# Performance work log

Measured on AMD Instinct MI355X. Metric: run time of the kernel, lower is better.

## Reference

```python
import jax, jax.numpy as jnp
import numpy as np

B, C, H, W = 1, 256, 48, 64
HW = H * W
HIDDEN, CTX = 128, 64
LEVELS, RADIUS = 4, 4
WIN = 2 * RADIUS + 1
P = WIN * WIN                     # 81 lookup points per level
CORR_DIM = P * LEVELS             # 324
TOP_K = 3
ITERS = 4
STEP_ROT, STEP_TRANS = 0.02, 0.02


def _sample_templates():
    # 12 directions x 3 scales + identity = 37 pose perturbations (as in __init__)
    base = [([0,0,0],[1,0,0]),([0,0,0],[-1,0,0]),([0,0,0],[0,1,0]),([0,0,0],[0,-1,0]),
            ([0,0,0],[0,0,1]),([0,0,0],[0,0,-1]),([1,0,0],[0,0,0]),([-1,0,0],[0,0,0]),
            ([0,1,0],[0,0,0]),([0,-1,0],[0,0,0]),([0,0,1],[0,0,0]),([0,0,-1],[0,0,0])]
    scales = np.array([0.25, 1.0, 4.0], np.float32)
    rot = np.repeat(np.array([r for r, _ in base], np.float32), 3, axis=0)
    trs = np.repeat(np.array([t for _, t in base], np.float32), 3, axis=0)
    sc = np.tile(scales, 12)
    axes = rot / np.clip(np.linalg.norm(rot, axis=1, keepdims=True), 1e-8, None)
    ha = STEP_ROT * sc / 2.0
    dq = np.stack([np.cos(ha), axes[:, 0]*np.sin(ha), axes[:, 1]*np.sin(ha), axes[:, 2]*np.sin(ha)], -1)
    dt = trs * (STEP_TRANS * sc[:, None])
    dq = np.concatenate([dq, [[1., 0., 0., 0.]]], 0)
    dt = np.concatenate([dt, [[0., 0., 0.]]], 0)
    return jnp.asarray(dq), jnp.asarray(dt)

DQ, DT = _sample_templates()     # (37,4), (37,3)
N_SAMPLES = DQ.shape[0]


def qmul(q, r):
    w1, x1, y1, z1 = jnp.moveaxis(q, -1, 0)
    w2, x2, y2, z2 = jnp.moveaxis(r, -1, 0)
    return jnp.stack([w1*w2 - x1*x2 - y1*y2 - z1*z2,
                      w1*x2 + x1*w2 + y1*z2 - z1*y2,
                      w1*y2 - x1*z2 + y1*w2 + z1*x2,
                      w1*z2 + x1*y2 - y1*x2 + z1*w2], -1)


def qapply(q, v):
    qv = jnp.concatenate([jnp.zeros(v.shape[:-1] + (1,), v.dtype), v], -1)
    qc = q * jnp.array([1., -1., -1., -1.], q.dtype)
    return qmul(qmul(q, qv), qc)[..., 1:]


def quat_to_R(q):
    w, x, y, z = jnp.moveaxis(q, -1, 0)
    R = jnp.stack([1-2*(y*y+z*z), 2*(x*y-w*z), 2*(x*z+w*y),
                   2*(x*y+w*z), 1-2*(x*x+z*z), 2*(y*z-w*x),
                   2*(x*z-w*y), 2*(y*z+w*x), 1-2*(x*x+y*y)], -1)
    return R.reshape(q.shape[:-1] + (3, 3))


def conv3(x, w, b):
    y = jax.lax.conv_general_dilated(x, w, (1, 1), 'SAME',
                                     dimension_numbers=('NCHW', 'OIHW', 'NCHW'))
    return y + b[None, :, None, None]


def bilinear_lookup(corr_flat, Hl, Wl, x, y):
    # corr_flat: (B,HW,Hl*Wl); x,y: (B,N,HW,P) -> (B,N,HW,P), zero padding outside
    x0 = jnp.floor(x)
    y0 = jnp.floor(y)
    out = jnp.zeros(x.shape, corr_flat.dtype)
    def gather(idx):
        g = lambda ix: jnp.take_along_axis(corr_flat, ix, axis=-1)
        return jax.vmap(g, in_axes=1, out_axes=1)(idx)   # vmap over N, no corr copy
    for dx_, dy_ in ((0, 0), (1, 0), (0, 1), (1, 1)):
        xi = x0 + dx_
        yi = y0 + dy_
        wgt = (1 - jnp.abs(x - xi)) * (1 - jnp.abs(y - yi))
        valid = (xi >= 0) & (xi < Wl) & (yi >= 0) & (yi < Hl)
        idx = (jnp.clip(yi, 0, Hl - 1) * Wl + jnp.clip(xi, 0, Wl - 1)).astype(jnp.int32)
        out = out + jnp.where(valid, wgt, 0.0) * gather(idx)
    return out


def _forward(fmap_rgb, fmap_depth, depth, context, intrinsics,
             Wz, bz, Wr, br, Wq, bq, Wh, bh, Wfc, bfc):
    f32 = jnp.float32
    fx = 60. + 40. * intrinsics[:, 0]
    fy = 60. + 40. * intrinsics[:, 1]
    cx = W / 2. + 4. * (intrinsics[:, 2] - 0.5)
    cy = H / 2. + 4. * (intrinsics[:, 3] - 0.5)
    d = 4.0 + 20.0 * depth                                  # (B,H,W) metric depth

    # 4D correlation pyramid: corr[b,i,:,:] = <fmap_depth pixel i, fmap_rgb>
    fd = fmap_depth.reshape(B, C, HW).transpose(0, 2, 1)    # (B,HW,C)
    corr = jnp.einsum('bic,bchw->bihw', fd, fmap_rgb) / jnp.sqrt(f32(C))
    pyramid = []
    cl, Hl, Wl = corr, H, W
    for _ in range(LEVELS):
        pyramid.append((cl.reshape(B, HW, Hl * Wl), Hl, Wl))
        cl = cl.reshape(B, HW, Hl // 2, 2, Wl // 2, 2).mean(axis=(3, 5))
        Hl //= 2
        Wl //= 2

    # back-projected depth points (B,HW,3)
    vv, uu = jnp.meshgrid(jnp.arange(H, dtype=f32), jnp.arange(W, dtype=f32), indexing='ij')
    uu = uu.reshape(HW)
    vv = vv.reshape(HW)
    df = d.reshape(B, HW)
    X = jnp.stack([(uu[None] - cx[:, None]) / fx[:, None] * df,
                   (vv[None] - cy[:, None]) / fy[:, None] * df, df], -1)

    off = jnp.arange(-RADIUS, RADIUS + 1, dtype=f32)
    oy, ox = jnp.meshgrid(off, off, indexing='ij')
    ox = ox.reshape(P)
    oy = oy.reshape(P)

    pose = jnp.tile(jnp.array([1., 0., 0., 0., 0., 0., 0.], f32)[None, :], (B, 1))
    h = jnp.zeros((B, HIDDEN, H, W), f32)

    for _ in range(ITERS):
        qc, tc = pose[:, :4], pose[:, 4:7]
        quats = qmul(qc[:, None, :], DQ[None])              # (B,N,4)
        quats = quats / jnp.linalg.norm(quats, axis=-1, keepdims=True)
        trans = tc[:, None, :] + qapply(qc[:, None, :], DT[None])
        Rm = quat_to_R(quats)                               # (B,N,3,3)
        Xc = jnp.einsum('bnij,bpj->bnpi', Rm, X) + trans[:, :, None, :]
        z = jnp.clip(Xc[..., 2], 0.1, None)
        u = fx[:, None, None] * Xc[..., 0] / z + cx[:, None, None]   # (B,N,HW)
        v = fy[:, None, None] * Xc[..., 1] / z + cy[:, None, None]
        feats = []
        for lvl, (cfl, Hl_, Wl_) in enumerate(pyramid):
            s = f32(2 ** lvl)
            xl = u[..., None] / s + ox
            yl = v[..., None] / s + oy
            feats.append(bilinear_lookup(cfl, Hl_, Wl_, xl, yl))
        cf = jnp.concatenate(feats, -1)                     # (B,N,HW,CORR_DIM)
        conf = cf.mean(axis=(2, 3))                         # (B,N) sample confidence
        topv, topi = jax.lax.top_k(conf, TOP_K)
        wk = jax.nn.softmax(topv, axis=-1)                  # confidence-weighted top-K
        idx = jnp.broadcast_to(topi[:, :, None, None], (B, TOP_K, HW, CORR_DIM))
        sel = jnp.take_along_axis(cf, idx, axis=1)
        fused = (wk[:, :, None, None] * sel).sum(1)         # (B,HW,CORR_DIM)
        fused = fused.transpose(0, 2, 1).reshape(B, CORR_DIM, H, W)

        # ConvGRU update
        x_in = jnp.concatenate([fused, context], 1)
        hx = jnp.concatenate([h, x_in], 1)
        zg = jax.nn.sigmoid(conv3(hx, Wz, bz))
        rg = jax.nn.sigmoid(conv3(hx, Wr, br))
        qg = jnp.tanh(conv3(jnp.concatenate([rg * h, x_in], 1), Wq, bq))
        h = (1 - zg) * h + zg * qg

        # 7D pose delta head + quaternion/Lie-style update
        feat = jax.nn.relu(conv3(h, Wh, bh)).mean(axis=(2, 3))
        delta = 0.01 * (feat @ Wfc + bfc)                   # (B,7)
        dq = jnp.concatenate([1.0 + delta[:, :1], delta[:, 1:4]], -1)
        dq = dq / jnp.linalg.norm(dq, axis=-1, keepdims=True)
        tn = tc + qapply(qc, delta[:, 4:7])
        qn = qmul(qc, dq)
        qn = qn / jnp.linalg.norm(qn, axis=-1, keepdims=True)
        pose = jnp.concatenate([qn, tn], -1)
    return pose


def setup_inputs() -> dict:
    key = jax.random.key(0)
    ks = jax.random.split(key, 12)
    rn = lambda k, shape, s=1.0: s * jax.random.normal(k, shape, jnp.float32)
    Gin = HIDDEN + CORR_DIM + CTX
    sc = 1.0 / np.sqrt(Gin * 9)
    sh = 1.0 / np.sqrt(HIDDEN * 9)
    return {
        'fmap_rgb': rn(ks[0], (B, C, H, W)),
        'fmap_depth': rn(ks[1], (B, C, H, W)),
        'depth': jax.random.uniform(ks[2], (B, H, W), jnp.float32),
        'context': rn(ks[3], (B, CTX, H, W)),
        'intrinsics': jax.random.uniform(ks[4], (B, 4), jnp.float32),
        'Wz': rn(ks[5], (HIDDEN, Gin, 3, 3), sc), 'bz': jnp.zeros((HIDDEN,), jnp.float32),
        'Wr': rn(ks[6], (HIDDEN, Gin, 3, 3), sc), 'br': jnp.zeros((HIDDEN,), jnp.float32),
        'Wq': rn(ks[7], (HIDDEN, Gin, 3, 3), sc), 'bq': jnp.zeros((HIDDEN,), jnp.float32),
        'Wh': rn(ks[8], (HIDDEN, HIDDEN, 3, 3), sh), 'bh': jnp.zeros((HIDDEN,), jnp.float32),
        'Wfc': rn(ks[9], (HIDDEN, 7), 1.0 / np.sqrt(HIDDEN)), 'bfc': jnp.zeros((7,), jnp.float32),
    }


def reference(fmap_rgb, fmap_depth, depth, context, intrinsics,
              Wz, bz, Wr, br, Wq, bq, Wh, bh, Wfc, bfc):
    return _forward(fmap_rgb, fmap_depth, depth, context, intrinsics,
                    Wz, bz, Wr, br, Wq, bq, Wh, bh, Wfc, bfc)
```

## Files before the change

### kernel.cpp

```cpp
#include <hip/hip_runtime.h>
#include <math.h>

constexpr int kH = 48, kW = 64, kHW = 3072, kC = 256;
constexpr int kHidden = 128, kCtx = 64;
constexpr int kP = 81, kCorrDim = 324;
constexpr int kNS = 37, kIters = 4;
constexpr int kGin = kHidden + kCorrDim + kCtx;
constexpr int kCinPad = 544;
constexpr int kStepsBig = 17 * 9;
constexpr int kStepsH = 4 * 9;

constexpr int kSB0 = 0, kSB1 = 4292, kSB2 = 5720, kSB3 = 6292, kSBTot = 6580;
constexpr int kHB0 = 0, kHB1 = 3552, kHB2 = 4560, kHB3 = 4872, kHBTot = 4980;

constexpr size_t U_CORR0 = 0;
constexpr size_t U_CORR1 = U_CORR0 + (size_t)kHW * 3072;
constexpr size_t U_CORR2 = U_CORR1 + (size_t)kHW * 768;
constexpr size_t U_CORR3 = U_CORR2 + (size_t)kHW * 192;
constexpr size_t U_END0  = U_CORR3 + (size_t)kHW * 48;
constexpr size_t F_X     = U_END0 / 2;
constexpr size_t F_H     = F_X + (size_t)kHW * 3;
constexpr size_t F_ZPRE  = F_H + (size_t)kHidden * kHW;
constexpr size_t F_END1  = F_ZPRE + (size_t)kHidden * kHW;
constexpr size_t U_BUFT  = F_END1 * 2;
constexpr size_t U_RHT   = U_BUFT + (size_t)kHW * kCinPad;
constexpr size_t U_PZR   = U_RHT + (size_t)kHW * kHidden;
constexpr size_t U_PQ    = U_PZR + (size_t)kStepsBig * 256 * 32;
constexpr size_t U_PH    = U_PQ + (size_t)kStepsBig * 128 * 32;
constexpr size_t U_END2  = U_PH + (size_t)kStepsH * 128 * 32;
constexpr size_t F_BZR   = (U_END2 + 2) / 2;
constexpr size_t F_CONF  = F_BZR + 256;
constexpr size_t F_TK    = F_CONF + 64;
constexpr size_t F_POSE  = F_TK + 16;
constexpr size_t F_FEAT  = F_POSE + 16;
constexpr size_t F_END3  = F_FEAT + 128;
constexpr size_t U_FDT   = F_END3 * 2;
constexpr size_t U_QT    = U_FDT + (size_t)kHW * kC;
constexpr size_t U_SBOX  = U_FDT;

typedef __attribute__((ext_vector_type(8))) short short8;
typedef __attribute__((ext_vector_type(4))) float f32x4;

__device__ inline unsigned short f2b(float f) {
  unsigned int u = __float_as_uint(f);
  unsigned int r = u + 0x7FFF + ((u >> 16) & 1);
  return (unsigned short)(r >> 16);
}
__device__ inline float b2f(unsigned short u) {
  return __uint_as_float(((unsigned int)u) << 16);
}
__device__ inline int clampi(int v, int lo, int hi) { return min(max(v, lo), hi); }

__constant__ float c_rot[12][3] = {
  {0,0,0},{0,0,0},{0,0,0},{0,0,0},{0,0,0},{0,0,0},
  {1,0,0},{-1,0,0},{0,1,0},{0,-1,0},{0,0,1},{0,0,-1}};
__constant__ float c_trs[12][3] = {
  {1,0,0},{-1,0,0},{0,1,0},{0,-1,0},{0,0,1},{0,0,-1},
  {0,0,0},{0,0,0},{0,0,0},{0,0,0},{0,0,0},{0,0,0}};

__device__ inline void d_qmul(const float* q, const float* r, float* o) {
  o[0] = q[0]*r[0] - q[1]*r[1] - q[2]*r[2] - q[3]*r[3];
  o[1] = q[0]*r[1] + q[1]*r[0] + q[2]*r[3] - q[3]*r[2];
  o[2] = q[0]*r[2] - q[1]*r[3] + q[2]*r[0] + q[3]*r[1];
  o[3] = q[0]*r[3] + q[1]*r[2] - q[2]*r[1] + q[3]*r[0];
}
__device__ inline void d_qapply(const float* q, const float* v, float* o) {
  float a0 = -q[1]*v[0] - q[2]*v[1] - q[3]*v[2];
  float a1 =  q[0]*v[0] + q[2]*v[2] - q[3]*v[1];
  float a2 =  q[0]*v[1] - q[1]*v[2] + q[3]*v[0];
  float a3 =  q[0]*v[2] + q[1]*v[1] - q[2]*v[0];
  o[0] = -a0*q[1] + a1*q[0] - a2*q[3] + a3*q[2];
  o[1] = -a0*q[2] + a1*q[3] + a2*q[0] - a3*q[1];
  o[2] = -a0*q[3] - a1*q[2] + a2*q[1] + a3*q[0];
}
__device__ inline void d_intr(const float* intr, float& fx, float& fy, float& cx, float& cy) {
  fx = 60.f + 40.f*intr[0];
  fy = 60.f + 40.f*intr[1];
  cx = 32.f + 4.f*(intr[2] - 0.5f);
  cy = 24.f + 4.f*(intr[3] - 0.5f);
}
__device__ inline void sample_Rt(int t, const float* __restrict__ pose, float* S) {
  float qc[4] = {pose[0], pose[1], pose[2], pose[3]};
  float tc[3] = {pose[4], pose[5], pose[6]};
  float dq[4], dt[3];
  if (t == 36) {
    dq[0] = 1.f; dq[1] = dq[2] = dq[3] = 0.f;
    dt[0] = dt[1] = dt[2] = 0.f;
  } else {
    int j = t / 3, k = t % 3;
    float sc = (k == 0) ? 0.25f : ((k == 1) ? 1.f : 4.f);
    float rx = c_rot[j][0], ry = c_rot[j][1], rz = c_rot[j][2];
    float nrm = sqrtf(rx*rx + ry*ry + rz*rz);
    float axn = fmaxf(nrm, 1e-8f);
    float ax = rx / axn, ay = ry / axn, az = rz / axn;
    float ha = 0.02f * sc * 0.5f;
    float sh = sinf(ha), ch = cosf(ha);
    dq[0] = ch; dq[1] = ax * sh; dq[2] = ay * sh; dq[3] = az * sh;
    dt[0] = c_trs[j][0] * (0.02f * sc);
    dt[1] = c_trs[j][1] * (0.02f * sc);
    dt[2] = c_trs[j][2] * (0.02f * sc);
  }
  float qn[4];
  d_qmul(qc, dq, qn);
  float inv = 1.f / sqrtf(qn[0]*qn[0] + qn[1]*qn[1] + qn[2]*qn[2] + qn[3]*qn[3]);
  qn[0] *= inv; qn[1] *= inv; qn[2] *= inv; qn[3] *= inv;
  float tr[3];
  d_qapply(qc, dt, tr);
  float w = qn[0], x = qn[1], y = qn[2], z = qn[3];
  S[0] = 1.f - 2.f*(y*y + z*z); S[1] = 2.f*(x*y - w*z);       S[2] = 2.f*(x*z + w*y);
  S[3] = 2.f*(x*y + w*z);       S[4] = 1.f - 2.f*(x*x + z*z); S[5] = 2.f*(y*z - w*x);
  S[6] = 2.f*(x*z - w*y);       S[7] = 2.f*(y*z + w*x);       S[8] = 1.f - 2.f*(x*x + y*y);
  S[9]  = tc[0] + tr[0];
  S[10] = tc[1] + tr[1];
  S[11] = tc[2] + tr[2];
}
__device__ inline void project_uv(const float* S, const float* Xp, const float* intr,
                                  float& u, float& v) {
  float xc0 = S[0]*Xp[0] + S[1]*Xp[1] + S[2]*Xp[2] + S[9];
  float xc1 = S[3]*Xp[0] + S[4]*Xp[1] + S[5]*Xp[2] + S[10];
  float xc2 = S[6]*Xp[0] + S[7]*Xp[1] + S[8]*Xp[2] + S[11];
  float z = fmaxf(xc2, 0.1f);
  float fx, fy, cx, cy;
  d_intr(intr, fx, fy, cx, cy);
  u = fx * xc0 / z + cx;
  v = fy * xc1 / z + cy;
}

__global__ void init_k(const float* __restrict__ ctx, const float* __restrict__ bz,
                       const float* __restrict__ br, const float* __restrict__ depth,
                       const float* __restrict__ intr, float* __restrict__ h,
                       unsigned short* __restrict__ bufT, float* __restrict__ bzr,
                       float* __restrict__ X, float* __restrict__ conf,
                       float* __restrict__ feat, float* __restrict__ pose) {
  int idx = blockIdx.x * blockDim.x + threadIdx.x;
  if (idx < kHidden * kHW) {
    h[idx] = 0.f;
    int p = idx >> 7, c = idx & 127;
    bufT[(size_t)p * kCinPad + c] = 0;
  }
  if (idx < kHW * 92) {
    int p = idx / 92, c = idx % 92;
    unsigned short v = 0;
    if (c < 64) v = f2b(ctx[(size_t)c * kHW + p]);
    bufT[(size_t)p * kCinPad + 452 + c] = v;
  }
  if (idx < kHW) {
    float fx, fy, cx, cy;
    d_intr(intr, fx, fy, cx, cy);
    float d = 4.f + 20.f * depth[idx];
    float u = (float)(idx % kW), v = (float)(idx / kW);
    X[idx*3+0] = (u - cx) / fx * d;
    X[idx*3+1] = (v - cy) / fy * d;
    X[idx*3+2] = d;
  }
  if (idx < 256) bzr[idx] = (idx < 128) ? bz[idx] : br[idx - 128];
  if (idx < 64) conf[idx] = 0.f;
  if (idx < 128) feat[idx] = 0.f;
  if (idx == 0) {
    pose[0] = 1.f;
    for (int j = 1; j < 7; ++j) pose[j] = 0.f;
  }
}

__global__ void pack_k(const float* __restrict__ W0, const float* __restrict__ W1,
                       int ocSplit, int OC, int nsteps, int nchunks, int Cin,
                       unsigned short* __restrict__ P) {
  int idx = blockIdx.x * blockDim.x + threadIdx.x;
  int total = nsteps * OC * 4;
  if (idx >= total) return;
  int g = idx & 3;
  int oc = (idx >> 2) % OC;
  int s = idx / (OC * 4);
  int tap = s / nchunks, cc = s % nchunks;
  union { unsigned short u[8]; uint4 q; } v;
#pragma unroll
  for (int j = 0; j < 8; ++j) {
    int ci = cc * 32 + g * 8 + j;
    float w = 0.f;
    if (ci < Cin)
      w = (oc < ocSplit) ? W0[((size_t)oc * Cin + ci) * 9 + tap]
                         : W1[((size_t)(oc - ocSplit) * Cin + ci) * 9 + tap];
    v.u[j] = f2b(w);
  }
  *(uint4*)&P[(size_t)idx * 8] = v.q;
}

__global__ __launch_bounds__(256) void t_bf16_k(const float* __restrict__ src,
                                                unsigned short* __restrict__ dst) {
  __shared__ float t[64][65];
  const int tid = threadIdx.x;
  const int p0 = blockIdx.x * 64, c0 = blockIdx.y * 64;
  const int tx = tid & 63, ty = tid >> 6;
  for (int cl = ty; cl < 64; cl += 4)
    t[cl][tx] = src[(size_t)(c0 + cl) * kHW + p0 + tx];
  __syncthreads();
  for (int pl = ty; pl < 64; pl += 4)
    dst[(size_t)(p0 + pl) * kC + c0 + tx] = f2b(t[tx][pl]);
}

__global__ __launch_bounds__(256) void corr_mfma_k(const unsigned short* __restrict__ fdT,
                                                   const unsigned short* __restrict__ qT,
                                                   unsigned short* __restrict__ Cg) {
  const int tid = threadIdx.x;
  const int wv = tid >> 6, lane = tid & 63;
  const int m = lane & 15, kg = lane >> 4;
  const int i0 = blockIdx.y * 128 + wv * 32;
  const int q0 = blockIdx.x * 128;

  f32x4 acc[2][8];
#pragma unroll
  for (int t = 0; t < 2; ++t)
#pragma unroll
    for (int u = 0; u < 8; ++u) acc[t][u] = (f32x4){0.f, 0.f, 0.f, 0.f};

#pragma unroll
  for (int kc = 0; kc < 8; ++kc) {
    const int kb = kc * 32 + kg * 8;
    short8 a[2], b[8];
#pragma unroll
    for (int t = 0; t < 2; ++t)
      a[t] = *(const short8*)&fdT[(size_t)(i0 + t * 16 + m) * kC + kb];
#pragma unroll
    for (int u = 0; u < 8; ++u)
      b[u] = *(const short8*)&qT[(size_t)(q0 + u * 16 + m) * kC + kb];
#pragma unroll
    for (int t = 0; t < 2; ++t)
#pragma unroll
      for (int u = 0; u < 8; ++u)
        acc[t][u] = __builtin_amdgcn_mfma_f32_16x16x32_bf16(a[t], b[u], acc[t][u], 0, 0, 0);
  }
  const float S = 0.0625f;
#pragma unroll
  for (int t = 0; t < 2; ++t)
#pragma unroll
    for (int u = 0; u < 8; ++u)
#pragma unroll
      for (int r = 0; r < 4; ++r)
        Cg[(size_t)(i0 + t * 16 + kg * 4 + r) * kHW + q0 + u * 16 + m] = f2b(acc[t][u][r] * S);
}

__global__ void pool2_k(const unsigned short* __restrict__ in,
                        unsigned short* __restrict__ out, int Hi, int Wi) {
  int Ho = Hi / 2, Wo = Wi / 2;
  int total = kHW * Ho * Wo;
  int idx = blockIdx.x * blockDim.x + threadIdx.x;
  if (idx >= total) return;
  int i = idx / (Ho * Wo);
  int r = idx % (Ho * Wo);
  int y = r / Wo, x = r % Wo;
  const unsigned short* p = in + (size_t)i * Hi * Wi;
  float v = 0.25f * (b2f(p[(2*y)*Wi + 2*x]) + b2f(p[(2*y)*Wi + 2*x + 1]) +
                     b2f(p[(2*y+1)*Wi + 2*x]) + b2f(p[(2*y+1)*Wi + 2*x + 1]));
  out[idx] = f2b(v);
}

__global__ __launch_bounds__(256) void boxbuild_k(const unsigned short* __restrict__ corr0,
                                                  const unsigned short* __restrict__ corr1,
                                                  const unsigned short* __restrict__ corr2,
                                                  const unsigned short* __restrict__ corr3,
                                                  unsigned short* __restrict__ Sbox) {
  __shared__ float pyr[4080];
  __shared__ float hb[kHBTot];
  const int i = blockIdx.x;
  const int tid = threadIdx.x;

  for (int idx = tid; idx < 4080; idx += 256) {
    float v;
    if (idx < 3072)      v = b2f(corr0[(size_t)i * 3072 + idx]);
    else if (idx < 3840) v = b2f(corr1[(size_t)i * 768 + idx - 3072]);
    else if (idx < 4032) v = b2f(corr2[(size_t)i * 192 + idx - 3840]);
    else                 v = b2f(corr3[(size_t)i * 48 + idx - 4032]);
    pyr[idx] = v;
  }
  __syncthreads();

  const int lvl_off[4] = {0, 3072, 3840, 4032};
  for (int c = tid; c < kHBTot; c += 256) {
    int lvl, rem;
    if (c < kHB1)      { lvl = 0; rem = c; }
    else if (c < kHB2) { lvl = 1; rem = c - kHB1; }
    else if (c < kHB3) { lvl = 2; rem = c - kHB2; }
    else               { lvl = 3; rem = c - kHB3; }
    const int Wl = kW >> lvl, Wp = Wl + 10;
    const int y = rem / Wp, as = rem % Wp;
    const float* row = &pyr[lvl_off[lvl] + y * Wl];
    const int x0 = max(0, as - 9), x1 = min(Wl - 1, as - 1);
    float s = 0.f;
    for (int x = x0; x <= x1; ++x) s += row[x];
    hb[c] = s;
  }
  __syncthreads();

  const int hoff[4] = {kHB0, kHB1, kHB2, kHB3};
  unsigned short* out = Sbox + (size_t)i * kSBTot;
  for (int c = tid; c < kSBTot; c += 256) {
    int lvl, rem;
    if (c < kSB1)      { lvl = 0; rem = c; }
    else if (c < kSB2) { lvl = 1; rem = c - kSB1; }
    else if (c < kSB3) { lvl = 2; rem = c - kSB2; }
    else               { lvl = 3; rem = c - kSB3; }
    const int Wl = kW >> lvl, Hl = kH >> lvl, Wp = Wl + 10;
    const int bp = rem / Wp, as = rem % Wp;
    const float* col = &hb[hoff[lvl] + as];
    const int r0 = max(0, bp - 9), r1 = min(Hl - 1, bp - 1);
    float s = 0.f;
    for (int r = r0; r <= r1; ++r) s += col[r * Wp];
    out[c] = f2b(s);
  }
}

__global__ __launch_bounds__(256) void conf_k(const unsigned short* __restrict__ Sbox,
                                              const float* __restrict__ X,
                                              const float* __restrict__ pose,
                                              const float* __restrict__ intr,
                                              float* __restrict__ conf) {
  const int idx = blockIdx.x * 256 + threadIdx.x;
  const int n = idx / kHW, i = idx - n * kHW;
  float S[12];
  sample_Rt(n, pose, S);
  float Xp[3] = {X[i*3], X[i*3+1], X[i*3+2]};
  float u, v;
  project_uv(S, Xp, intr, u, v);
  const unsigned short* sb = Sbox + (size_t)i * kSBTot;
  float tot = 0.f;
#pragma unroll
  for (int l = 0; l < 4; ++l) {
    const int Wp = (kW >> l) + 10, Hp = (kH >> l) + 10;
    const int so = (l == 0) ? kSB0 : (l == 1) ? kSB1 : (l == 2) ? kSB2 : kSB3;
    const float s = (float)(1 << l);
    const float bx = u / s, by = v / s;
    const float fbx = floorf(bx), fby = floorf(by);
    const int x0 = (int)fbx, y0 = (int)fby;
    const float fx = bx - fbx, fy = by - fby;
    const int xa = clampi(x0 + 5, 0, Wp - 1), xb = clampi(x0 + 6, 0, Wp - 1);
    const int ya = clampi(y0 + 5, 0, Hp - 1), yb = clampi(y0 + 6, 0, Hp - 1);
    const float s00 = b2f(sb[so + ya * Wp + xa]), s10 = b2f(sb[so + ya * Wp + xb]);
    const float s01 = b2f(sb[so + yb * Wp + xa]), s11 = b2f(sb[so + yb * Wp + xb]);
    tot += (1.f - fx) * (1.f - fy) * s00 + fx * (1.f - fy) * s10 +
           (1.f - fx) * fy * s01 + fx * fy * s11;
  }
#pragma unroll
  for (int o = 32; o; o >>= 1) tot += __shfl_xor(tot, o, 64);
  if ((threadIdx.x & 63) == 0) atomicAdd(&conf[n], tot);
}

__global__ void topk_k(float* __restrict__ conf, float* __restrict__ tkw,
                       int* __restrict__ tki) {
  if (threadIdx.x != 0) return;
  const float scale = 1.f / ((float)kHW * (float)kCorrDim);
  float c[kNS];
  for (int n = 0; n < kNS; ++n) c[n] = conf[n] * scale;
  int id[3] = {-1, -1, -1};
  float v[3];
  for (int k = 0; k < 3; ++k) {
    float best = -1e30f;
    int bi = -1;
    for (int n = 0; n < kNS; ++n) {
      if (n == id[0] || n == id[1] || n == id[2]) continue;
      if (c[n] > best) { best = c[n]; bi = n; }
    }
    v[k] = best;
    id[k] = bi;
  }
  float m = v[0];
  float e0 = expf(v[0] - m), e1 = expf(v[1] - m), e2 = expf(v[2] - m);
  float s = e0 + e1 + e2;
  tkw[0] = e0 / s; tkw[1] = e1 / s; tkw[2] = e2 / s;
  tki[0] = id[0]; tki[1] = id[1]; tki[2] = id[2];
  for (int n = 0; n < kNS; ++n) conf[n] = 0.f;
}

__global__ __launch_bounds__(256) void fused_k(const unsigned short* __restrict__ corr0,
                                               const unsigned short* __restrict__ corr1,
                                               const unsigned short* __restrict__ corr2,
                                               const unsigned short* __restrict__ corr3,
                                               const float* __restrict__ X,
                                               const float* __restrict__ pose,
                                               const float* __restrict__ intr,
                                               const float* __restrict__ tkw,
                                               const int* __restrict__ tki,
                                               unsigned short* __restrict__ bufT) {
  __shared__ float win[12][10][12];
  __shared__ float s_fx[12], s_fy[12];
  __shared__ int   s_ix[12], s_iy[12];
  __shared__ float s_w[3];
  const int i = blockIdx.x;
  const int tid = threadIdx.x;

  if (tid < 3) {
    int n = tki[tid];
    s_w[tid] = tkw[tid];
    float S[12];
    sample_Rt(n, pose, S);
    float Xp[3] = {X[i*3], X[i*3+1], X[i*3+2]};
    float u, v;
    project_uv(S, Xp, intr, u, v);
#pragma unroll
    for (int l = 0; l < 4; ++l) {
      float s = (float)(1 << l);
      float bx = u / s, by = v / s;
      float fbx = floorf(bx), fby = floorf(by);
      s_ix[tid*4 + l] = (int)fbx;
      s_iy[tid*4 + l] = (int)fby;
      s_fx[tid*4 + l] = bx - fbx;
      s_fy[tid*4 + l] = by - fby;
    }
  }
  __syncthreads();

  for (int sidx = tid; sidx < 1200; sidx += 256) {
    const int w = sidx / 100, rem = sidx % 100;
    const int rr = rem / 10, cc = rem % 10;
    const int lvl = w & 3;
    const int Wl = kW >> lvl, Hl = kH >> lvl;
    const unsigned short* base =
        (lvl == 0) ? corr0 : (lvl == 1) ? corr1 : (lvl == 2) ? corr2 : corr3;
    const int y = s_iy[w] - 4 + rr;
    const int x = s_ix[w] - 4 + cc;
    float v = 0.f;
    if (y >= 0 && y < Hl && x >= 0 && x < Wl)
      v = b2f(base[(size_t)i * (Hl * Wl) + y * Wl + x]);
    win[w][rr][cc] = v;
  }
  __syncthreads();

  for (int d = tid; d < kCorrDim; d += 256) {
    const int lvl = d / kP;
    const int o = d % kP;
    const int oyi = o / 9, oxi = o % 9;
    float val = 0.f;
#pragma unroll
    for (int k = 0; k < 3; ++k) {
      const int w = k * 4 + lvl;
      const float fx = s_fx[w], fy = s_fy[w];
      const float w00 = (1.f - fx) * (1.f - fy), w10 = fx * (1.f - fy);
      const float w01 = (1.f - fx) * fy, w11 = fx * fy;
      val += s_w[k] * (w00 * win[w][oyi][oxi] + w10 * win[w][oyi][oxi + 1] +
                       w01 * win[w][oyi + 1][oxi] + w11 * win[w][oyi + 1][oxi + 1]);
    }
    bufT[(size_t)i * kCinPad + kHidden + d] = f2b(val);
  }
}

template<int OC, int NCH, bool QMODE>
__device__ inline void conv_kloop(const unsigned short* __restrict__ inT,
                                  const unsigned short* __restrict__ rhT,
                                  const unsigned short* __restrict__ P,
                                  int y, int wv, int lane, int ocBlock,
                                  f32x4 (&acc)[2][2]) {
  const int m = lane & 15, kg = lane >> 4;
  const int ocW = ocBlock + (wv >> 1) * 32;
  const int pxW = (wv & 1) * 32;
#pragma unroll
  for (int tap = 0; tap < 9; ++tap) {
    const int dy = tap / 3 - 1, dx = tap % 3 - 1;
    const int yy = y + dy;
    if (yy < 0 || yy >= kH) continue;
    const int xs0 = pxW + m + dx, xs1 = pxW + 16 + m + dx;
    const bool v0 = (xs0 >= 0) && (xs0 < kW);
    const bool v1 = (xs1 >= 0) && (xs1 < kW);
    const int px0 = yy * kW + xs0, px1 = yy * kW + xs1;
    const unsigned short* a_base = P + ((size_t)(tap * NCH) * OC + ocW + m) * 32 + kg * 8;
#pragma unroll
    for (int cc = 0; cc < NCH; ++cc) {
      const unsigned short* srcB;
      int stride;
      if (QMODE && cc < 4) { srcB = rhT; stride = kHidden; }
      else                 { srcB = inT; stride = kCinPad; }
      short8 a0 = *(const short8*)(a_base + (size_t)cc * OC * 32);
      short8 a1 = *(const short8*)(a_base + (size_t)cc * OC * 32 + 16 * 32);
      short8 b0 = {0, 0, 0, 0, 0, 0, 0, 0};
      short8 b1 = {0, 0, 0, 0, 0, 0, 0, 0};
      if (v0) b0 = *(const short8*)(srcB + (size_t)px0 * stride + cc * 32 + kg * 8);
      if (v1) b1 = *(const short8*)(srcB + (size_t)px1 * stride + cc * 32 + kg * 8);
      acc[0][0] = __builtin_amdgcn_mfma_f32_16x16x32_bf16(a0, b0, acc[0][0], 0, 0, 0);
      acc[0][1] = __builtin_amdgcn_mfma_f32_16x16x32_bf16(a0, b1, acc[0][1], 0, 0, 0);
      acc[1][0] = __builtin_amdgcn_mfma_f32_16x16x32_bf16(a1, b0, acc[1][0], 0, 0, 0);
      acc[1][1] = __builtin_amdgcn_mfma_f32_16x16x32_bf16(a1, b1, acc[1][1], 0, 0, 0);
    }
  }
}

__global__ __launch_bounds__(256) void conv_zr_k(const unsigned short* __restrict__ bufT,
                                                 const unsigned short* __restrict__ P,
                                                 const float* __restrict__ bzr,
                                                 float* __restrict__ zpre,
                                                 const float* __restrict__ hbuf,
                                                 unsigned short* __restrict__ rhT) {
  const int tid = threadIdx.x;
  const int wv = tid >> 6, lane = tid & 63;
  const int y = blockIdx.y, ocBlock = blockIdx.x * 64;
  f32x4 acc[2][2] = {{{0.f,0.f,0.f,0.f},{0.f,0.f,0.f,0.f}},
                     {{0.f,0.f,0.f,0.f},{0.f,0.f,0.f,0.f}}};
  conv_kloop<256, 17, false>(bufT, nullptr, P, y, wv, lane, ocBlock, acc);
  const int m = lane & 15, kg = lane >> 4;
  const int ocW = ocBlock + (wv >> 1) * 32, pxW = (wv & 1) * 32;
#pragma unroll
  for (int ot = 0; ot < 2; ++ot)
#pragma unroll
    for (int t = 0; t < 2; ++t)
#pragma unroll
      for (int r = 0; r < 4; ++r) {
        const int oc = ocW + ot * 16 + kg * 4 + r;
        const int px = y * kW + pxW + t * 16 + m;
        const float val = acc[ot][t][r] + bzr[oc];
        if (oc < kHidden) {
          zpre[(size_t)oc * kHW + px] = val;
        } else {
          const float rg = 1.f / (1.f + expf(-val));
          rhT[(size_t)px * kHidden + oc - kHidden] = f2b(rg * hbuf[(size_t)(oc - kHidden) * kHW + px]);
        }
      }
}

__global__ __launch_bounds__(256) void conv_q_k(unsigned short* __restrict__ bufT,
                                                const unsigned short* __restrict__ rhT,
                                                const unsigned short* __restrict__ P,
                                                const float* __restrict__ bq,
                                                const float* __restrict__ zpre,
                                                float* __restrict__ hbuf) {
  const int tid = threadIdx.x;
  const int wv = tid >> 6, lane = tid & 63;
  const int y = blockIdx.y, ocBlock = blockIdx.x * 64;
  f32x4 acc[2][2] = {{{0.f,0.f,0.f,0.f},{0.f,0.f,0.f,0.f}},
                     {{0.f,0.f,0.f,0.f},{0.f,0.f,0.f,0.f}}};
  conv_kloop<128, 17, true>(bufT, rhT, P, y, wv, lane, ocBlock, acc);
  const int m = lane & 15, kg = lane >> 4;
  const int ocW = ocBlock + (wv >> 1) * 32, pxW = (wv & 1) * 32;
#pragma unroll
  for (int ot = 0; ot < 2; ++ot)
#pragma unroll
    for (int t = 0; t < 2; ++t)
#pragma unroll
      for (int r = 0; r < 4; ++r) {
        const int oc = ocW + ot * 16 + kg * 4 + r;
        const int px = y * kW + pxW + t * 16 + m;
        const size_t off = (size_t)oc * kHW + px;
        const float q = acc[ot][t][r] + bq[oc];
        const float zg = 1.f / (1.f + expf(-zpre[off]));
        const float hn = (1.f - zg) * hbuf[off] + zg * tanhf(q);
        hbuf[off] = hn;
        bufT[(size_t)px * kCinPad + oc] = f2b(hn);
      }
}

__global__ __launch_bounds__(256) void conv_h_k(const unsigned short* __restrict__ bufT,
                                                const unsigned short* __restrict__ P,
                                                const float* __restrict__ bh,
                                                float* __restrict__ feat) {
  __shared__ float fb[64];
  const int tid = threadIdx.x;
  const int wv = tid >> 6, lane = tid & 63;
  const int y = blockIdx.y, ocBlock = blockIdx.x * 64;
  f32x4 acc[2][2] = {{{0.f,0.f,0.f,0.f},{0.f,0.f,0.f,0.f}},
                     {{0.f,0.f,0.f,0.f},{0.f,0.f,0.f,0.f}}};
  conv_kloop<128, 4, false>(bufT, nullptr, P, y, wv, lane, ocBlock, acc);
  if (tid < 64) fb[tid] = 0.f;
  __syncthreads();
  const int m = lane & 15, kg = lane >> 4;
  const int ocW = ocBlock + (wv >> 1) * 32;
#pragma unroll
  for (int ot = 0; ot < 2; ++ot)
#pragma unroll
    for (int r = 0; r < 4; ++r) {
      const int oc = ocW + ot * 16 + kg * 4 + r;
      const float bv = bh[oc];
      float v = fmaxf(acc[ot][0][r] + bv, 0.f) + fmaxf(acc[ot][1][r] + bv, 0.f);
      v += __shfl_xor(v, 1, 64);
      v += __shfl_xor(v, 2, 64);
      v += __shfl_xor(v, 4, 64);
      v += __shfl_xor(v, 8, 64);
      if (m == 0) atomicAdd(&fb[oc - ocBlock], v);
    }
  __syncthreads();
  if (tid < 64) atomicAdd(&feat[ocBlock + tid], fb[tid]);
}

__global__ void pose_update_k(float* __restrict__ feat, const float* __restrict__ Wfc,
                              const float* __restrict__ bfc, float* __restrict__ pose,
                              float* __restrict__ out) {
  __shared__ float s_d[7];
  int t = threadIdx.x;
  if (t < 7) {
    float s = 0.f;
    const float inv = 1.f / (float)kHW;
    for (int k = 0; k < kHidden; ++k) s += (feat[k] * inv) * Wfc[k * 7 + t];
    s_d[t] = 0.01f * (s + bfc[t]);
  }
  __syncthreads();
  if (t < kHidden) feat[t] = 0.f;
  if (t != 0) return;
  float qc[4] = {pose[0], pose[1], pose[2], pose[3]};
  float tc[3] = {pose[4], pose[5], pose[6]};
  float dq[4] = {1.f + s_d[0], s_d[1], s_d[2], s_d[3]};
  float inv = 1.f / sqrtf(dq[0]*dq[0] + dq[1]*dq[1] + dq[2]*dq[2] + dq[3]*dq[3]);
  dq[0] *= inv; dq[1] *= inv; dq[2] *= inv; dq[3] *= inv;
  float dv[3] = {s_d[4], s_d[5], s_d[6]};
  float rv[3];
  d_qapply(qc, dv, rv);
  float tn[3] = {tc[0] + rv[0], tc[1] + rv[1], tc[2] + rv[2]};
  float qn[4];
  d_qmul(qc, dq, qn);
  float inv2 = 1.f / sqrtf(qn[0]*qn[0] + qn[1]*qn[1] + qn[2]*qn[2] + qn[3]*qn[3]);
  qn[0] *= inv2; qn[1] *= inv2; qn[2] *= inv2; qn[3] *= inv2;
  pose[0] = qn[0]; pose[1] = qn[1]; pose[2] = qn[2]; pose[3] = qn[3];
  pose[4] = tn[0]; pose[5] = tn[1]; pose[6] = tn[2];
  out[0] = qn[0]; out[1] = qn[1]; out[2] = qn[2]; out[3] = qn[3];
  out[4] = tn[0]; out[5] = tn[1]; out[6] = tn[2];
}

extern "C" void kernel_launch(void* const* d_in, const int* in_sizes, int n_in,
                              void* d_out, int out_size, void* d_ws, size_t ws_size,
                              hipStream_t stream) {
  const float* frgb  = (const float*)d_in[0];
  const float* fdep  = (const float*)d_in[1];
  const float* depth = (const float*)d_in[2];
  const float* ctx   = (const float*)d_in[3];
  const float* intr  = (const float*)d_in[4];
  const float* Wz = (const float*)d_in[5];
  const float* bz = (const float*)d_in[6];
  const float* Wr = (const float*)d_in[7];
  const float* br = (const float*)d_in[8];
  const float* Wq = (const float*)d_in[9];
  const float* bq = (const float*)d_in[10];
  const float* Wh = (const float*)d_in[11];
  const float* bh = (const float*)d_in[12];
  const float* Wfc = (const float*)d_in[13];
  const float* bfc = (const float*)d_in[14];
  float* outp = (float*)d_out;

  float* ws = (float*)d_ws;
  unsigned short* us = (unsigned short*)d_ws;
  unsigned short* corr0 = us + U_CORR0;
  unsigned short* corr1 = us + U_CORR1;
  unsigned short* corr2 = us + U_CORR2;
  unsigned short* corr3 = us + U_CORR3;
  float* X    = ws + F_X;
  float* hbuf = ws + F_H;
  float* zpre = ws + F_ZPRE;
  unsigned short* bufT = us + U_BUFT;
  unsigned short* rhT  = us + U_RHT;
  unsigned short* Pzr  = us + U_PZR;
  unsigned short* Pq   = us + U_PQ;
  unsigned short* Ph   = us + U_PH;
  float* bzr  = ws + F_BZR;
  float* conf = ws + F_CONF;
  float* tkw  = ws + F_TK;
  int*   tki  = (int*)(ws + F_TK + 3);
  float* pose = ws + F_POSE;
  float* feat = ws + F_FEAT;
  unsigned short* fdT  = us + U_FDT;
  unsigned short* qT   = us + U_QT;
  unsigned short* Sbox = us + U_SBOX;

  init_k<<<1536, 256, 0, stream>>>(ctx, bz, br, depth, intr, hbuf, bufT, bzr, X,
                                   conf, feat, pose);
  pack_k<<<(kStepsBig * 256 * 4 + 255) / 256, 256, 0, stream>>>(Wz, Wr, 128, 256,
                                                                kStepsBig, 17, kGin, Pzr);
  pack_k<<<(kStepsBig * 128 * 4 + 255) / 256, 256, 0, stream>>>(Wq, Wq, 128, 128,
                                                                kStepsBig, 17, kGin, Pq);
  pack_k<<<(kStepsH * 128 * 4 + 255) / 256, 256, 0, stream>>>(Wh, Wh, 128, 128,
                                                              kStepsH, 4, kHidden, Ph);
  t_bf16_k<<<dim3(48, 4), 256, 0, stream>>>(fdep, fdT);
  t_bf16_k<<<dim3(48, 4), 256, 0, stream>>>(frgb, qT);
  corr_mfma_k<<<dim3(24, 24), 256, 0, stream>>>(fdT, qT, corr0);
  {
    int t1 = kHW * 24 * 32, t2 = kHW * 12 * 16, t3 = kHW * 6 * 8;
    pool2_k<<<(t1 + 255) / 256, 256, 0, stream>>>(corr0, corr1, 48, 64);
    pool2_k<<<(t2 + 255) / 256, 256, 0, stream>>>(corr1, corr2, 24, 32);
    pool2_k<<<(t3 + 255) / 256, 256, 0, stream>>>(corr2, corr3, 12, 16);
  }
  boxbuild_k<<<kHW, 256, 0, stream>>>(corr0, corr1, corr2, corr3, Sbox);

  for (int it = 0; it < kIters; ++it) {
    conf_k<<<444, 256, 0, stream>>>(Sbox, X, pose, intr, conf);
    topk_k<<<1, 64, 0, stream>>>(conf, tkw, tki);
    fused_k<<<kHW, 256, 0, stream>>>(corr0, corr1, corr2, corr3, X, pose, intr,
                                     tkw, tki, bufT);
    conv_zr_k<<<dim3(4, 48), 256, 0, stream>>>(bufT, Pzr, bzr, zpre, hbuf, rhT);
    conv_q_k<<<dim3(2, 48), 256, 0, stream>>>(bufT, rhT, Pq, bq, zpre, hbuf);
    conv_h_k<<<dim3(2, 48), 256, 0, stream>>>(bufT, Ph, bh, feat);
    pose_update_k<<<1, 128, 0, stream>>>(feat, Wfc, bfc, pose, outp);
  }
}
```

Baseline: 904.0 us.

## Stage conv tiles in LDS and use prefix sums for box sums

The three GRU convolution kernels now stage, for each 32-channel chunk, a 3x66 halo tile of input pixels and the matching 9-tap weight slice into shared memory before running the MFMA loop. Previously each tap re-read activations and weights from global memory. Separately, the box-filter builder replaces its explicit 9-wide window loops with row prefix scans (wave shuffles) and column prefix sums, so each box sum becomes a difference of two reads. The costs are extra barriers per channel chunk, roughly 58KB of LDS per block (which limits occupancy), and possible bf16/fp32 cancellation error from the prefix differences.

```diff
diff --git a/kernel.cpp b/kernel.cpp
--- a/kernel.cpp
+++ b/kernel.cpp
@@ -254,6 +254,19 @@
   out[idx] = f2b(v);
 }
 
+template<int HL>
+__device__ inline void colpref(float* base, int Wp) {
+  float v[HL];
+#pragma unroll
+  for (int y = 0; y < HL; ++y) v[y] = base[(size_t)y * Wp];
+  float run = 0.f;
+#pragma unroll
+  for (int y = 0; y < HL; ++y) {
+    run += v[y];
+    base[(size_t)y * Wp] = run;
+  }
+}
+
 __global__ __launch_bounds__(256) void boxbuild_k(const unsigned short* __restrict__ corr0,
                                                   const unsigned short* __restrict__ corr1,
                                                   const unsigned short* __restrict__ corr2,
@@ -263,6 +276,7 @@
   __shared__ float hb[kHBTot];
   const int i = blockIdx.x;
   const int tid = threadIdx.x;
+  const int wv = tid >> 6, lane = tid & 63;
 
   for (int idx = tid; idx < 4080; idx += 256) {
     float v;
@@ -275,6 +289,24 @@
   __syncthreads();
 
   const int lvl_off[4] = {0, 3072, 3840, 4032};
+  for (int r = wv; r < 90; r += 4) {
+    int lvl, y;
+    if (r < 48)      { lvl = 0; y = r; }
+    else if (r < 72) { lvl = 1; y = r - 48; }
+    else if (r < 84) { lvl = 2; y = r - 72; }
+    else             { lvl = 3; y = r - 84; }
+    const int Wl = kW >> lvl;
+    float* row = &pyr[lvl_off[lvl] + y * Wl];
+    float v = (lane < Wl) ? row[lane] : 0.f;
+#pragma unroll
+    for (int o = 1; o < 64; o <<= 1) {
+      float tv = __shfl_up(v, o, 64);
+      if (lane >= o) v += tv;
+    }
+    if (lane < Wl) row[lane] = v;
+  }
+  __syncthreads();
+
   for (int c = tid; c < kHBTot; c += 256) {
     int lvl, rem;
     if (c < kHB1)      { lvl = 0; rem = c; }
@@ -283,15 +315,23 @@
     else               { lvl = 3; rem = c - kHB3; }
     const int Wl = kW >> lvl, Wp = Wl + 10;
     const int y = rem / Wp, as = rem % Wp;
-    const float* row = &pyr[lvl_off[lvl] + y * Wl];
-    const int x0 = max(0, as - 9), x1 = min(Wl - 1, as - 1);
-    float s = 0.f;
-    for (int x = x0; x <= x1; ++x) s += row[x];
-    hb[c] = s;
+    const float* pref = &pyr[lvl_off[lvl] + y * Wl];
+    float Hv = 0.f;
+    if (as >= 1) Hv = pref[min(Wl - 1, as - 1)];
+    if (as >= 10) Hv -= pref[as - 10];
+    hb[c] = Hv;
   }
   __syncthreads();
 
   const int hoff[4] = {kHB0, kHB1, kHB2, kHB3};
+  if (tid < 160) {
+    if (tid < 74)       colpref<48>(hb + kHB0 + tid, 74);
+    else if (tid < 116) colpref<24>(hb + kHB1 + (tid - 74), 42);
+    else if (tid < 142) colpref<12>(hb + kHB2 + (tid - 116), 26);
+    else                colpref<6>(hb + kHB3 + (tid - 142), 18);
+  }
+  __syncthreads();
+
   unsigned short* out = Sbox + (size_t)i * kSBTot;
   for (int c = tid; c < kSBTot; c += 256) {
     int lvl, rem;
@@ -302,10 +342,10 @@
     const int Wl = kW >> lvl, Hl = kH >> lvl, Wp = Wl + 10;
     const int bp = rem / Wp, as = rem % Wp;
     const float* col = &hb[hoff[lvl] + as];
-    const int r0 = max(0, bp - 9), r1 = min(Hl - 1, bp - 1);
-    float s = 0.f;
-    for (int r = r0; r <= r1; ++r) s += col[r * Wp];
-    out[c] = f2b(s);
+    float S = 0.f;
+    if (bp >= 1) S = col[(size_t)min(Hl - 1, bp - 1) * Wp];
+    if (bp >= 10) S -= col[(size_t)(bp - 10) * Wp];
+    out[c] = f2b(S);
   }
 }
 
@@ -442,37 +482,48 @@
   }
 }
 
-template<int OC, int NCH, bool QMODE>
-__device__ inline void conv_kloop(const unsigned short* __restrict__ inT,
-                                  const unsigned short* __restrict__ rhT,
-                                  const unsigned short* __restrict__ P,
-                                  int y, int wv, int lane, int ocBlock,
-                                  f32x4 (&acc)[2][2]) {
-  const int m = lane & 15, kg = lane >> 4;
-  const int ocW = ocBlock + (wv >> 1) * 32;
-  const int pxW = (wv & 1) * 32;
-#pragma unroll
-  for (int tap = 0; tap < 9; ++tap) {
-    const int dy = tap / 3 - 1, dx = tap % 3 - 1;
-    const int yy = y + dy;
-    if (yy < 0 || yy >= kH) continue;
-    const int xs0 = pxW + m + dx, xs1 = pxW + 16 + m + dx;
-    const bool v0 = (xs0 >= 0) && (xs0 < kW);
-    const bool v1 = (xs1 >= 0) && (xs1 < kW);
-    const int px0 = yy * kW + xs0, px1 = yy * kW + xs1;
-    const unsigned short* a_base = P + ((size_t)(tap * NCH) * OC + ocW + m) * 32 + kg * 8;
-#pragma unroll
-    for (int cc = 0; cc < NCH; ++cc) {
-      const unsigned short* srcB;
-      int stride;
-      if (QMODE && cc < 4) { srcB = rhT; stride = kHidden; }
-      else                 { srcB = inT; stride = kCinPad; }
-      short8 a0 = *(const short8*)(a_base + (size_t)cc * OC * 32);
-      short8 a1 = *(const short8*)(a_base + (size_t)cc * OC * 32 + 16 * 32);
-      short8 b0 = {0, 0, 0, 0, 0, 0, 0, 0};
-      short8 b1 = {0, 0, 0, 0, 0, 0, 0, 0};
-      if (v0) b0 = *(const short8*)(srcB + (size_t)px0 * stride + cc * 32 + kg * 8);
-      if (v1) b1 = *(const short8*)(srcB + (size_t)px1 * stride + cc * 32 + kg * 8);
+template<bool QMODE>
+__device__ inline void conv_core(unsigned short* Bs, unsigned short* As,
+                                 const unsigned short* __restrict__ inT,
+                                 const unsigned short* __restrict__ rhT,
+                                 const unsigned short* __restrict__ P,
+                                 int y, int tid, int ocBase, int OC, int NCH,
+                                 f32x4 (&acc)[2][2]) {
+  const int wv = tid >> 6, lane = tid & 63;
+  const int n = lane & 15, kg = lane >> 4;
+  const int oc0 = (wv >> 1) * 32, px0 = (wv & 1) * 32;
+
+  for (int cc = 0; cc < NCH; ++cc) {
+    __syncthreads();
+    for (int idx2 = tid; idx2 < 792; idx2 += 256) {
+      const int g = idx2 & 3;
+      const int xx = (idx2 >> 2) % 66;
+      const int r = (idx2 >> 2) / 66;
+      const int gy = y + r - 1, gx = xx - 1;
+      uint4 val = {0, 0, 0, 0};
+      if (gy >= 0 && gy < kH && gx >= 0 && gx < kW) {
+        if (QMODE && cc < 4)
+          val = *(const uint4*)&rhT[(size_t)(gy * kW + gx) * kHidden + cc * 32 + g * 8];
+        else
+          val = *(const uint4*)&inT[(size_t)(gy * kW + gx) * kCinPad + cc * 32 + g * 8];
+      }
+      *(uint4*)&Bs[(r * 66 + xx) * 40 + g * 8] = val;
+    }
+    for (int idx3 = tid; idx3 < 2304; idx3 += 256) {
+      const int tap = idx3 >> 8;
+      const int rem = idx3 & 255;
+      const int ocl = rem >> 2, g = rem & 3;
+      uint4 av = *(const uint4*)&P[(((size_t)(tap * NCH + cc) * OC + ocBase + ocl) * 4 + g) * 8];
+      *(uint4*)&As[(tap * 64 + ocl) * 40 + g * 8] = av;
+    }
+    __syncthreads();
+#pragma unroll
+    for (int tap = 0; tap < 9; ++tap) {
+      const int ky = tap / 3, kx = tap % 3;
+      short8 a0 = *(const short8*)&As[(tap * 64 + oc0 + n) * 40 + kg * 8];
+      short8 a1 = *(const short8*)&As[(tap * 64 + oc0 + 16 + n) * 40 + kg * 8];
+      short8 b0 = *(const short8*)&Bs[(ky * 66 + px0 + n + kx) * 40 + kg * 8];
+      short8 b1 = *(const short8*)&Bs[(ky * 66 + px0 + 16 + n + kx) * 40 + kg * 8];
       acc[0][0] = __builtin_amdgcn_mfma_f32_16x16x32_bf16(a0, b0, acc[0][0], 0, 0, 0);
       acc[0][1] = __builtin_amdgcn_mfma_f32_16x16x32_bf16(a0, b1, acc[0][1], 0, 0, 0);
       acc[1][0] = __builtin_amdgcn_mfma_f32_16x16x32_bf16(a1, b0, acc[1][0], 0, 0, 0);
@@ -487,14 +538,16 @@
                                                  float* __restrict__ zpre,
                                                  const float* __restrict__ hbuf,
                                                  unsigned short* __restrict__ rhT) {
+  __shared__ unsigned short Bs[3 * 66 * 40];
+  __shared__ unsigned short As[9 * 64 * 40];
   const int tid = threadIdx.x;
   const int wv = tid >> 6, lane = tid & 63;
-  const int y = blockIdx.y, ocBlock = blockIdx.x * 64;
+  const int y = blockIdx.y, ocBase = blockIdx.x * 64;
   f32x4 acc[2][2] = {{{0.f,0.f,0.f,0.f},{0.f,0.f,0.f,0.f}},
                      {{0.f,0.f,0.f,0.f},{0.f,0.f,0.f,0.f}}};
-  conv_kloop<256, 17, false>(bufT, nullptr, P, y, wv, lane, ocBlock, acc);
+  conv_core<false>(Bs, As, bufT, nullptr, P, y, tid, ocBase, 256, 17, acc);
   const int m = lane & 15, kg = lane >> 4;
-  const int ocW = ocBlock + (wv >> 1) * 32, pxW = (wv & 1) * 32;
+  const int ocW = ocBase + (wv >> 1) * 32, pxW = (wv & 1) * 32;
 #pragma unroll
   for (int ot = 0; ot < 2; ++ot)
 #pragma unroll
@@ -519,14 +572,16 @@
                                                 const float* __restrict__ bq,
                                                 const float* __restrict__ zpre,
                                                 float* __restrict__ hbuf) {
+  __shared__ unsigned short Bs[3 * 66 * 40];
+  __shared__ unsigned short As[9 * 64 * 40];
   const int tid = threadIdx.x;
   const int wv = tid >> 6, lane = tid & 63;
-  const int y = blockIdx.y, ocBlock = blockIdx.x * 64;
+  const int y = blockIdx.y, ocBase = blockIdx.x * 64;
   f32x4 acc[2][2] = {{{0.f,0.f,0.f,0.f},{0.f,0.f,0.f,0.f}},
                      {{0.f,0.f,0.f,0.f},{0.f,0.f,0.f,0.f}}};
-  conv_kloop<128, 17, true>(bufT, rhT, P, y, wv, lane, ocBlock, acc);
+  conv_core<true>(Bs, As, bufT, rhT, P, y, tid, ocBase, 128, 17, acc);
   const int m = lane & 15, kg = lane >> 4;
-  const int ocW = ocBlock + (wv >> 1) * 32, pxW = (wv & 1) * 32;
+  const int ocW = ocBase + (wv >> 1) * 32, pxW = (wv & 1) * 32;
 #pragma unroll
   for (int ot = 0; ot < 2; ++ot)
 #pragma unroll
@@ -548,17 +603,19 @@
                                                 const unsigned short* __restrict__ P,
                                                 const float* __restrict__ bh,
                                                 float* __restrict__ feat) {
+  __shared__ unsigned short Bs[3 * 66 * 40];
+  __shared__ unsigned short As[9 * 64 * 40];
   __shared__ float fb[64];
   const int tid = threadIdx.x;
   const int wv = tid >> 6, lane = tid & 63;
-  const int y = blockIdx.y, ocBlock = blockIdx.x * 64;
+  const int y = blockIdx.y, ocBase = blockIdx.x * 64;
   f32x4 acc[2][2] = {{{0.f,0.f,0.f,0.f},{0.f,0.f,0.f,0.f}},
                      {{0.f,0.f,0.f,0.f},{0.f,0.f,0.f,0.f}}};
-  conv_kloop<128, 4, false>(bufT, nullptr, P, y, wv, lane, ocBlock, acc);
+  conv_core<false>(Bs, As, bufT, nullptr, P, y, tid, ocBase, 128, 4, acc);
   if (tid < 64) fb[tid] = 0.f;
   __syncthreads();
   const int m = lane & 15, kg = lane >> 4;
-  const int ocW = ocBlock + (wv >> 1) * 32;
+  const int ocW = ocBase + (wv >> 1) * 32;
 #pragma unroll
   for (int ot = 0; ot < 2; ++ot)
 #pragma unroll
@@ -570,10 +627,10 @@
       v += __shfl_xor(v, 2, 64);
       v += __shfl_xor(v, 4, 64);
       v += __shfl_xor(v, 8, 64);
-      if (m == 0) atomicAdd(&fb[oc - ocBlock], v);
+      if (m == 0) atomicAdd(&fb[oc - ocBase], v);
     }
   __syncthreads();
-  if (tid < 64) atomicAdd(&feat[ocBlock + tid], fb[tid]);
+  if (tid < 64) atomicAdd(&feat[ocBase + tid], fb[tid]);
 }
 
 __global__ void pose_update_k(float* __restrict__ feat, const float* __restrict__ Wfc,
```

Result: slower. 1.101 ms (+21.8%).
